# Kernel tuning notes

Measured on AMD Instinct MI355X. Metric: run time of the kernel, lower is better.

## Reference

```python
import jax, jax.numpy as jnp
import numpy as np

CONF_THRES = 0.25
IOU_THRES = 0.45
MAX_DET = 100      # yolov5 max_det passed in forward()
K_PRE = 1024       # pre-NMS candidate cap (yolov5 uses 30000; capped for O(k^2) IoU)
MAX_WH = 7680.0    # yolov5 class-offset trick for non-agnostic NMS
EPS = 1e-7


def _xywh2xyxy(b):
    # b: [k, 4] (cx, cy, w, h) -> (x1, y1, x2, y2)
    cx, cy, w, h = b[:, 0], b[:, 1], b[:, 2], b[:, 3]
    return jnp.stack([cx - w * 0.5, cy - h * 0.5, cx + w * 0.5, cy + h * 0.5], axis=-1)


def _iou_matrix(boxes):
    # boxes: [k, 4] xyxy -> [k, k] pairwise IoU
    lt = jnp.maximum(boxes[:, None, :2], boxes[None, :, :2])
    rb = jnp.minimum(boxes[:, None, 2:], boxes[None, :, 2:])
    wh = jnp.clip(rb - lt, 0.0)
    inter = wh[..., 0] * wh[..., 1]
    area = (boxes[:, 2] - boxes[:, 0]) * (boxes[:, 3] - boxes[:, 1])
    union = area[:, None] + area[None, :] - inter
    return inter / (union + EPS)


def _nms_single(pred):
    # pred: [N, 5+nc] = (cx, cy, w, h, obj, cls...)
    obj = pred[:, 4]
    cls_conf = pred[:, 5:] * obj[:, None]          # obj * cls, yolov5 conf
    score = jnp.max(cls_conf, axis=-1)             # best-class score
    cls = jnp.argmax(cls_conf, axis=-1)
    valid = (obj > CONF_THRES) & (score > CONF_THRES)

    # top K_PRE candidates by score (invalid -> -1)
    s_masked = jnp.where(valid, score, -1.0)
    scores_t, idx = jax.lax.top_k(s_masked, K_PRE)  # sorted descending
    boxes = _xywh2xyxy(pred[idx, :4])               # [K_PRE, 4]
    cls_t = cls[idx].astype(pred.dtype)
    valid_t = scores_t > 0.0

    # class offset so different classes never overlap (agnostic=False)
    iou = _iou_matrix(boxes + cls_t[:, None] * MAX_WH)

    # greedy sequential suppression over score-sorted candidates
    idxr = jnp.arange(K_PRE)

    def step(keep, xs):
        i, iou_row = xs
        sup = jnp.any((iou_row > IOU_THRES) & keep & (idxr < i))
        keep = keep.at[i].set(keep[i] & ~sup)
        return keep, None

    keep, _ = jax.lax.scan(step, valid_t, (idxr, iou))

    # gather up to MAX_DET kept detections (already score-sorted)
    sk = jnp.where(keep, scores_t, -1.0)
    sel_scores, sel = jax.lax.top_k(sk, MAX_DET)
    det = jnp.concatenate(
        [boxes[sel], scores_t[sel][:, None], cls_t[sel][:, None]], axis=-1)  # [MAX_DET, 6]
    det = jnp.where((sel_scores > 0.0)[:, None], det, 0.0)
    return det


def setup_inputs() -> dict:
    key = jax.random.key(0)
    B, N, C = 8, 100800, 85  # img_size=1280, 3 anchors, strides 8/16/32; nc=80
    pred = jax.random.uniform(key, (B, N, C), dtype=jnp.float32)
    # put box coords in pixel range [0, 640); scores stay in [0, 1)
    pred = pred.at[..., :4].multiply(640.0)
    return {"pred": pred}


def reference(pred) -> jnp.ndarray:
    # [B, MAX_DET, 6] = (x1, y1, x2, y2, conf, cls), zero-padded
    return jax.vmap(_nms_single)(pred)
```

## Files before the change

kernel.cpp:

```cpp
#include <hip/hip_runtime.h>
#include <hip/hip_bf16.h>

typedef unsigned int u32;
typedef unsigned long long u64;

#define B 8
#define NANCH 100800
#define NCH 85
#define KPRE 1024
#define MAXDET 100
#define CONF 0.25f
#define IOU_T 0.45f
#define EPS_F 1e-7f
#define MAX_WH 7680.0f
#define CAP 4096
#define NBIN 257
#define BASEBITS 0x3E800000u

#define ROWS 16
#define RDW 85
#define CHDW (ROWS * RDW)
#define CHF4 (CHDW / 4)
#define NCHUNK (B * NANCH / ROWS)
#define CPB (NANCH / ROWS)

__global__ __launch_bounds__(256, 5) void score_kernel(const float* __restrict__ pred,
                                                       u32* __restrict__ keys,
                                                       unsigned char* __restrict__ cls8,
                                                       u32* __restrict__ ghist) {
    __shared__ __align__(16) float sbuf[4 * CHDW];
    __shared__ u32 lh[B * NBIN];
    for (int i = threadIdx.x; i < B * NBIN; i += 256) lh[i] = 0;
    __syncthreads();

    const int lane = threadIdx.x & 63;
    const int wloc = threadIdx.x >> 6;
    const int q    = lane >> 4;
    const int r    = lane & 15;
    float* sw = &sbuf[wloc * CHDW];
    const int gwave = (blockIdx.x << 2) | wloc;
    const int nwaves = gridDim.x << 2;

    float4 a0, a1, a2, a3, a4, at;
    a0 = a1 = a2 = a3 = a4 = at = make_float4(0.f, 0.f, 0.f, 0.f);
    if (gwave < NCHUNK) {
        const float4* s4 = (const float4*)pred + (size_t)gwave * CHF4;
        a0 = s4[0 * 64 + lane];
        a1 = s4[1 * 64 + lane];
        a2 = s4[2 * 64 + lane];
        a3 = s4[3 * 64 + lane];
        a4 = s4[4 * 64 + lane];
        if (lane < 20) at = s4[320 + lane];
    }

    for (int ch = gwave; ch < NCHUNK; ch += nwaves) {
        int nx = ch + nwaves;
        float4 b0, b1, b2, b3, b4, bt;
        b0 = b1 = b2 = b3 = b4 = bt = make_float4(0.f, 0.f, 0.f, 0.f);
        if (nx < NCHUNK) {
            const float4* s4n = (const float4*)pred + (size_t)nx * CHF4;
            b0 = s4n[0 * 64 + lane];
            b1 = s4n[1 * 64 + lane];
            b2 = s4n[2 * 64 + lane];
            b3 = s4n[3 * 64 + lane];
            b4 = s4n[4 * 64 + lane];
            if (lane < 20) bt = s4n[320 + lane];
        }

        *(float4*)&sw[(0 * 64 + lane) * 4] = a0;
        *(float4*)&sw[(1 * 64 + lane) * 4] = a1;
        *(float4*)&sw[(2 * 64 + lane) * 4] = a2;
        *(float4*)&sw[(3 * 64 + lane) * 4] = a3;
        *(float4*)&sw[(4 * 64 + lane) * 4] = a4;
        if (lane < 20) *(float4*)&sw[(320 + lane) * 4] = at;

        const float* row = &sw[r * RDW];
        float obj = row[4];
        const float* cp = row + 5 + 20 * q;
        float best = -1.0f;
        int bidx = 0;
        #pragma unroll
        for (int c = 0; c < 20; ++c) {
            float v = cp[c] * obj;
            bool g = v > best;
            best = g ? v : best;
            bidx = g ? c : bidx;
        }
        bidx += 20 * q;

        float xo = __shfl_xor(best, 16);
        int io = __shfl_xor(bidx, 16);
        bool t = xo > best;
        best = t ? xo : best;
        bidx = t ? io : bidx;
        xo = __shfl_xor(best, 32);
        io = __shfl_xor(bidx, 32);
        t = xo > best;
        best = t ? xo : best;
        bidx = t ? io : bidx;

        if (lane < 16) {
            bool valid = (obj > CONF) & (best > CONF);
            u32 k = valid ? __float_as_uint(best) : 0u;
            int a = ch * ROWS + r;
            keys[a] = k;
            cls8[a] = (unsigned char)bidx;
            if (k) {
                int b = ch / CPB;
                u32 bin = (k - BASEBITS) >> 16;
                if (bin > 256) bin = 256;
                atomicAdd(&lh[b * NBIN + bin], 1u);
            }
        }

        a0 = b0; a1 = b1; a2 = b2; a3 = b3; a4 = b4; at = bt;
    }
    __syncthreads();
    for (int i = threadIdx.x; i < B * NBIN; i += 256) {
        u32 v = lh[i];
        if (v) atomicAdd(&ghist[i], v);
    }
}

__global__ __launch_bounds__(1024) void select_kernel(const float* __restrict__ pred,
                                                      const u32* __restrict__ keys,
                                                      const unsigned char* __restrict__ cls8,
                                                      const u32* __restrict__ ghist,
                                                      float* __restrict__ out) {
    #pragma clang fp contract(off)
    const int b = blockIdx.x;
    const int tid = threadIdx.x;

    __shared__ u64 items[CAP];
    __shared__ float s_score[KPRE];
    __shared__ float s_cls[KPRE];
    __shared__ float4 s_box[KPRE];
    __shared__ float4 s_obox[KPRE];
    __shared__ float s_area[KPRE];
    __shared__ u32 s_hist[NBIN];
    __shared__ int s_piv;
    __shared__ int s_cnt;
    __shared__ int s_keep[MAXDET];
    __shared__ int s_nk;

    if (tid < NBIN) s_hist[tid] = ghist[b * NBIN + tid];
    if (tid == 0) s_cnt = 0;
    __syncthreads();
    if (tid == 0) {
        int cum = 0, piv = 0;
        for (int t = 256; t >= 0; --t) {
            cum += (int)s_hist[t];
            if (cum >= KPRE) { piv = t; break; }
        }
        s_piv = piv;
    }
    __syncthreads();
    const int piv = s_piv;

    const uint4* kb4 = (const uint4*)(keys + (size_t)b * NANCH);
    const int NV = NANCH / 4;
    for (int j = tid; j < NV; j += 1024) {
        uint4 kv = kb4[j];
        u32 ks[4] = {kv.x, kv.y, kv.z, kv.w};
        #pragma unroll
        for (int e = 0; e < 4; ++e) {
            u32 k = ks[e];
            if (k) {
                u32 bin = (k - BASEBITS) >> 16;
                if (bin > 256) bin = 256;
                if ((int)bin >= piv) {
                    int p = atomicAdd(&s_cnt, 1);
                    if (p < CAP) items[p] = (((u64)(~k)) << 32) | (u32)(j * 4 + e);
                }
            }
        }
    }
    __syncthreads();
    int n = s_cnt; if (n > CAP) n = CAP;

    int m = KPRE;
    while (m < n) m <<= 1;
    for (int i = tid; i < m; i += 1024)
        if (i >= n) items[i] = ~0ull;
    __syncthreads();

    for (int k = 2; k <= m; k <<= 1) {
        for (int j = k >> 1; j >= 1; j >>= 1) {
            for (int p = tid; p < m / 2; p += 1024) {
                int i = ((p & ~(j - 1)) << 1) | (p & (j - 1));
                int pr = i | j;
                bool up = ((i & k) == 0);
                u64 a = items[i], c = items[pr];
                if ((a > c) == up) { items[i] = c; items[pr] = a; }
            }
            __syncthreads();
        }
    }

    if (tid < KPRE) {
        u64 it = items[tid];
        u32 invk = (u32)(it >> 32);
        if (invk != 0xFFFFFFFFu && tid < n) {
            u32 k = ~invk;
            u32 idx = (u32)it;
            float score = __uint_as_float(k);
            const float* pb = pred + ((size_t)b * NANCH + idx) * NCH;
            float cx = pb[0], cy = pb[1], w = pb[2], h = pb[3];
            float x1 = cx - w * 0.5f;
            float y1 = cy - h * 0.5f;
            float x2 = cx + w * 0.5f;
            float y2 = cy + h * 0.5f;
            float clsf = (float)cls8[(size_t)b * NANCH + idx];
            float off = clsf * MAX_WH;
            float bx1 = x1 + off, by1 = y1 + off, bx2 = x2 + off, by2 = y2 + off;
            s_score[tid] = score;
            s_cls[tid] = clsf;
            s_box[tid] = make_float4(x1, y1, x2, y2);
            s_obox[tid] = make_float4(bx1, by1, bx2, by2);
            s_area[tid] = (bx2 - bx1) * (by2 - by1);
        } else {
            s_score[tid] = -1.0f;
            s_cls[tid] = 0.0f;
            s_box[tid] = make_float4(0.f, 0.f, 0.f, 0.f);
            s_obox[tid] = make_float4(0.f, 0.f, 0.f, 0.f);
            s_area[tid] = 0.0f;
        }
    }
    __syncthreads();

    if (tid < 64) {
        const int lane = tid;
        float4 kb0 = make_float4(0, 0, 0, 0), kb1 = kb0;
        float ka0 = 0.0f, ka1 = 0.0f;
        int kept = 0;

        float sc_n = s_score[0];
        float4 cb_n = s_obox[0];
        float ca_n = s_area[0];

        for (int i = 0; i < KPRE; ++i) {
            float sc = sc_n;
            float4 cb = cb_n;
            float ca = ca_n;
            if (i + 1 < KPRE) {
                sc_n = s_score[i + 1];
                cb_n = s_obox[i + 1];
                ca_n = s_area[i + 1];
            }
            if (sc <= 0.0f) break;

            bool sup0 = false, sup1 = false;
            if (lane < kept) {
                float ltx = fmaxf(cb.x, kb0.x);
                float lty = fmaxf(cb.y, kb0.y);
                float rbx = fminf(cb.z, kb0.z);
                float rby = fminf(cb.w, kb0.w);
                float iw = fmaxf(rbx - ltx, 0.0f);
                float ih = fmaxf(rby - lty, 0.0f);
                float inter = iw * ih;
                float uni = ca + ka0 - inter;
                sup0 = (inter / (uni + EPS_F)) > IOU_T;
            }
            if (lane + 64 < kept) {
                float ltx = fmaxf(cb.x, kb1.x);
                float lty = fmaxf(cb.y, kb1.y);
                float rbx = fminf(cb.z, kb1.z);
                float rby = fminf(cb.w, kb1.w);
                float iw = fmaxf(rbx - ltx, 0.0f);
                float ih = fmaxf(rby - lty, 0.0f);
                float inter = iw * ih;
                float uni = ca + ka1 - inter;
                sup1 = (inter / (uni + EPS_F)) > IOU_T;
            }
            u64 bal = __ballot(sup0 || sup1);
            if (bal == 0) {
                if (lane == 0) s_keep[kept] = i;
                if (kept < 64) {
                    if (lane == kept) { kb0 = cb; ka0 = ca; }
                } else {
                    if (lane == kept - 64) { kb1 = cb; ka1 = ca; }
                }
                ++kept;
                if (kept >= MAXDET) break;
            }
        }
        if (lane == 0) s_nk = kept;
    }
    __syncthreads();
    const int nk = s_nk;

    if (tid < MAXDET) {
        float o0 = 0, o1 = 0, o2 = 0, o3 = 0, o4 = 0, o5 = 0;
        if (tid < nk) {
            int i = s_keep[tid];
            float4 bx = s_box[i];
            o0 = bx.x; o1 = bx.y; o2 = bx.z; o3 = bx.w;
            o4 = s_score[i];
            o5 = s_cls[i];
        }
        float* po = out + ((size_t)b * MAXDET + tid) * 6;
        po[0] = o0; po[1] = o1; po[2] = o2; po[3] = o3; po[4] = o4; po[5] = o5;
    }
}

extern "C" void kernel_launch(void* const* d_in, const int* in_sizes, int n_in,
                              void* d_out, int out_size, void* d_ws, size_t ws_size,
                              hipStream_t stream) {
    const float* pred = (const float*)d_in[0];
    float* out = (float*)d_out;
    char* ws = (char*)d_ws;

    u32* keys           = (u32*)(ws + 0);
    unsigned char* cls8 = (unsigned char*)(ws + 3225600);
    u32* ghist          = (u32*)(ws + 4032000);

    hipMemsetAsync(ghist, 0, B * NBIN * sizeof(u32), stream);
    score_kernel<<<1260, 256, 0, stream>>>(pred, keys, cls8, ghist);
    select_kernel<<<B, 1024, 0, stream>>>(pred, keys, cls8, ghist, out);
}
```

Before: 436.2 us.

## Split candidate filtering into a multi-block kernel before per-image NMS

Moves the threshold scan over each image's key array out of the 8-block select kernel into a separate 256-block filter kernel. Each block compacts the candidates of its slice into shared memory, then appends them to a per-image global buffer through an atomic counter. The NMS kernel then only loads the compacted candidates, so the 100800-key scan is no longer done by just 8 blocks. The cost is an extra launch and a global round trip for the candidates. Candidate order now depends on block scheduling, but the bitonic sort that follows makes the final result deterministic.

```diff
diff --git a/kernel.cpp b/kernel.cpp
--- a/kernel.cpp
+++ b/kernel.cpp
@@ -122,28 +122,19 @@
     }
 }
 
-__global__ __launch_bounds__(1024) void select_kernel(const float* __restrict__ pred,
-                                                      const u32* __restrict__ keys,
-                                                      const unsigned char* __restrict__ cls8,
-                                                      const u32* __restrict__ ghist,
-                                                      float* __restrict__ out) {
-    #pragma clang fp contract(off)
-    const int b = blockIdx.x;
+__global__ __launch_bounds__(256) void filter_kernel(const u32* __restrict__ keys,
+                                                     const u32* __restrict__ ghist,
+                                                     u32* __restrict__ gcnt,
+                                                     u64* __restrict__ gcand) {
+    __shared__ u64 sitems[4096];
+    __shared__ u32 s_hist[NBIN];
+    __shared__ int s_piv, s_cnt, s_base;
+
+    const int b = blockIdx.x >> 5;
+    const int g = blockIdx.x & 31;
     const int tid = threadIdx.x;
 
-    __shared__ u64 items[CAP];
-    __shared__ float s_score[KPRE];
-    __shared__ float s_cls[KPRE];
-    __shared__ float4 s_box[KPRE];
-    __shared__ float4 s_obox[KPRE];
-    __shared__ float s_area[KPRE];
-    __shared__ u32 s_hist[NBIN];
-    __shared__ int s_piv;
-    __shared__ int s_cnt;
-    __shared__ int s_keep[MAXDET];
-    __shared__ int s_nk;
-
-    if (tid < NBIN) s_hist[tid] = ghist[b * NBIN + tid];
+    for (int i = tid; i < NBIN; i += 256) s_hist[i] = ghist[b * NBIN + i];
     if (tid == 0) s_cnt = 0;
     __syncthreads();
     if (tid == 0) {
@@ -159,7 +150,7 @@
 
     const uint4* kb4 = (const uint4*)(keys + (size_t)b * NANCH);
     const int NV = NANCH / 4;
-    for (int j = tid; j < NV; j += 1024) {
+    for (int j = (g << 8) + tid; j < NV; j += 8192) {
         uint4 kv = kb4[j];
         u32 ks[4] = {kv.x, kv.y, kv.z, kv.w};
         #pragma unroll
@@ -170,13 +161,45 @@
                 if (bin > 256) bin = 256;
                 if ((int)bin >= piv) {
                     int p = atomicAdd(&s_cnt, 1);
-                    if (p < CAP) items[p] = (((u64)(~k)) << 32) | (u32)(j * 4 + e);
+                    if (p < 4096) sitems[p] = (((u64)(~k)) << 32) | (u32)(j * 4 + e);
                 }
             }
         }
     }
     __syncthreads();
-    int n = s_cnt; if (n > CAP) n = CAP;
+    int cnt = s_cnt; if (cnt > 4096) cnt = 4096;
+    if (tid == 0) s_base = (int)atomicAdd(&gcnt[b], (u32)cnt);
+    __syncthreads();
+    const int base = s_base;
+    u64* gout = gcand + (size_t)b * CAP;
+    for (int i = tid; i < cnt; i += 256) {
+        int pos = base + i;
+        if (pos < CAP) gout[pos] = sitems[i];
+    }
+}
+
+__global__ __launch_bounds__(1024) void selnms_kernel(const float* __restrict__ pred,
+                                                      const unsigned char* __restrict__ cls8,
+                                                      const u32* __restrict__ gcnt,
+                                                      const u64* __restrict__ gcand,
+                                                      float* __restrict__ out) {
+    #pragma clang fp contract(off)
+    const int b = blockIdx.x;
+    const int tid = threadIdx.x;
+
+    __shared__ u64 items[CAP];
+    __shared__ float s_score[KPRE];
+    __shared__ float s_cls[KPRE];
+    __shared__ float4 s_box[KPRE];
+    __shared__ float4 s_obox[KPRE];
+    __shared__ float s_area[KPRE];
+    __shared__ int s_keep[MAXDET];
+    __shared__ int s_nk;
+
+    int nq = (int)gcnt[b];
+    int n = nq > CAP ? CAP : nq;
+    const u64* gin = gcand + (size_t)b * CAP;
+    for (int i = tid; i < n; i += 1024) items[i] = gin[i];
 
     int m = KPRE;
     while (m < n) m <<= 1;
@@ -313,8 +336,11 @@
     u32* keys           = (u32*)(ws + 0);
     unsigned char* cls8 = (unsigned char*)(ws + 3225600);
     u32* ghist          = (u32*)(ws + 4032000);
-
-    hipMemsetAsync(ghist, 0, B * NBIN * sizeof(u32), stream);
+    u32* gcnt           = (u32*)(ws + 4040224);
+    u64* gcand          = (u64*)(ws + 4040256);
+
+    hipMemsetAsync(ghist, 0, B * NBIN * sizeof(u32) + B * sizeof(u32), stream);
     score_kernel<<<1260, 256, 0, stream>>>(pred, keys, cls8, ghist);
-    select_kernel<<<B, 1024, 0, stream>>>(pred, keys, cls8, ghist, out);
+    filter_kernel<<<256, 256, 0, stream>>>(keys, ghist, gcnt, gcand);
+    selnms_kernel<<<B, 1024, 0, stream>>>(pred, cls8, gcnt, gcand, out);
 }
```

Result: faster. 417.9 us (-4.2%).
